# Performance work log

Hardware: AMD Instinct MI355X
Metric: run time of the kernel (lower is better)

## Reference

```python
import jax, jax.numpy as jnp
import numpy as np

B, S, H = 4, 1024, 2048
E = 16            # num_experts
K = 2             # num_experts_per_token
I = 1024          # per-expert intermediate_dim
N_SHARED = 2
I_SHARED = I * N_SHARED
RATIO = 0.1       # shared_expert_ratio
EPS = 1e-9


def _swiglu(x, wg, wu, wd):
    # SwiGLU, bias=False: down( silu(gate(x)) * up(x) )
    return (jax.nn.silu(x @ wg) * (x @ wu)) @ wd


def setup_inputs() -> dict:
    key = jax.random.key(0)
    ks = jax.random.split(key, 9)
    scale = 0.02
    x = jax.random.normal(ks[0], (B, S, H), dtype=jnp.float32)
    centroids = jax.random.normal(ks[1], (E, H), dtype=jnp.float32)  # nn.Parameter(randn)
    gate_bias = jnp.zeros((E,), dtype=jnp.float32)
    # shared expert SwiGLU weights (intermediate = I * n_shared_experts)
    wg_s = jax.random.normal(ks[2], (H, I_SHARED), dtype=jnp.float32) * scale
    wu_s = jax.random.normal(ks[3], (H, I_SHARED), dtype=jnp.float32) * scale
    wd_s = jax.random.normal(ks[4], (I_SHARED, H), dtype=jnp.float32) * scale
    # routed experts, stacked [E, ...]
    wg = jax.random.normal(ks[5], (E, H, I), dtype=jnp.float32) * scale
    wu = jax.random.normal(ks[6], (E, H, I), dtype=jnp.float32) * scale
    wd = jax.random.normal(ks[7], (E, I, H), dtype=jnp.float32) * scale
    return {"x": x, "centroids": centroids, "gate_bias": gate_bias,
            "wg_s": wg_s, "wu_s": wu_s, "wd_s": wd_s,
            "wg": wg, "wu": wu, "wd": wd}


def reference(x, centroids, gate_bias, wg_s, wu_s, wd_s, wg, wu, wd):
    # 1) shared expert on ALL tokens, scaled by ratio
    shared = _swiglu(x, wg_s, wu_s, wd_s) * RATIO          # [B,S,H]
    # 2) centroid affinity (DeepSeek-V3 sigmoid gating)
    affinity = jax.nn.sigmoid(jnp.einsum('bsh,eh->bse', x, centroids))  # [B,S,E]
    # 3) bias used ONLY for selection
    biased = affinity + gate_bias
    _, top_idx = jax.lax.top_k(biased, K)                  # [B,S,K]
    # 4) clean weights from unbiased affinity, normalized to sum 1
    top_aff = jnp.take_along_axis(affinity, top_idx, axis=-1)  # [B,S,K]
    weights = top_aff / (top_aff.sum(-1, keepdims=True) + EPS)
    # 5) combine-mask: per-token per-expert weight (0 if not selected)
    mask = (jax.nn.one_hot(top_idx, E, dtype=x.dtype) * weights[..., None]).sum(-2)  # [B,S,E]
    # 6) expert compute + weighted combine; loop over fixed small E avoids
    #    materializing a [B,S,E,H] tensor
    routed = jnp.zeros_like(x)
    for e in range(E):
        routed = routed + mask[..., e:e + 1] * _swiglu(x, wg[e], wu[e], wd[e])
    return shared + routed
```

## Files before the change

kernel.cpp:

```cpp
#include <hip/hip_runtime.h>
#include <hip/hip_bf16.h>

typedef unsigned short u16;
typedef unsigned int u32;
typedef unsigned long long u64;
typedef __attribute__((ext_vector_type(8))) short short8;
typedef __attribute__((ext_vector_type(4))) float f32x4;

#define TOKENS 4096
#define HDIM 2048
#define NEXP 16
#define IDIM 1024
#define ISH 2048
#define MAXTILES 80
#define NCHUNK 128

#define AS1(p) ((const __attribute__((address_space(1))) u32*)(p))
#define AS3(p) ((__attribute__((address_space(3))) u32*)(p))

__device__ __forceinline__ u16 f2b(float f) {
    u32 u = __float_as_uint(f);
    u32 r = u + 0x7fffu + ((u >> 16) & 1u);
    return (u16)(r >> 16);
}

__global__ __launch_bounds__(256) void convert_x_kernel(const float* __restrict__ x,
                                                        u16* __restrict__ xb) {
    size_t i = ((size_t)blockIdx.x * 256 + threadIdx.x) * 8;
    float4 a = *(const float4*)(x + i);
    float4 b = *(const float4*)(x + i + 4);
    u32 p0 = (u32)f2b(a.x) | ((u32)f2b(a.y) << 16);
    u32 p1 = (u32)f2b(a.z) | ((u32)f2b(a.w) << 16);
    u32 p2 = (u32)f2b(b.x) | ((u32)f2b(b.y) << 16);
    u32 p3 = (u32)f2b(b.z) | ((u32)f2b(b.w) << 16);
    uint4 o = make_uint4(p0, p1, p2, p3);
    *(uint4*)(xb + i) = o;
}

__global__ __launch_bounds__(256) void route_kernel(const float* __restrict__ x,
                                                    const float* __restrict__ cent,
                                                    const float* __restrict__ bias,
                                                    int* __restrict__ top_e,
                                                    float* __restrict__ top_w) {
    __shared__ alignas(16) float cs[8 * 2048];
    int lane = threadIdx.x & 63;
    int wv = threadIdx.x >> 6;
    int t = blockIdx.x * 4 + wv;
    const float4* xp4 = (const float4*)(x + (size_t)t * HDIM);
    float4 xr[8];
#pragma unroll
    for (int i = 0; i < 8; i++) xr[i] = xp4[lane + 64 * i];
    float aff[16];
#pragma unroll
    for (int ph = 0; ph < 2; ph++) {
        if (ph) __syncthreads();
        const float* sbase = cent + (size_t)(ph * 8 + wv * 2) * HDIM;
        float* dbase = cs + (size_t)wv * 2 * HDIM;
#pragma unroll
        for (int i = 0; i < 16; i++) {
            __builtin_amdgcn_global_load_lds(AS1(sbase + i * 256 + lane * 4),
                                             AS3(dbase + i * 256), 16, 0, 0);
        }
        __syncthreads();
#pragma unroll
        for (int e = 0; e < 8; e++) {
            const float4* cp = (const float4*)cs + (size_t)e * 512;
            float s = 0.f;
#pragma unroll
            for (int i = 0; i < 8; i++) {
                float4 cv = cp[lane + 64 * i];
                s += xr[i].x * cv.x;
                s += xr[i].y * cv.y;
                s += xr[i].z * cv.z;
                s += xr[i].w * cv.w;
            }
#pragma unroll
            for (int off = 32; off > 0; off >>= 1) s += __shfl_xor(s, off, 64);
            aff[ph * 8 + e] = 1.f / (1.f + expf(-s));
        }
    }
    float b0 = -1e30f, b1 = -1e30f, a0 = 0.f, a1 = 0.f;
    int e0 = -1, e1 = -1;
#pragma unroll
    for (int e = 0; e < 16; e++) {
        float v = aff[e] + bias[e];
        if (v > b0) {
            b1 = b0; e1 = e0; a1 = a0;
            b0 = v; e0 = e; a0 = aff[e];
        } else if (v > b1) {
            b1 = v; e1 = e; a1 = aff[e];
        }
    }
    float inv = 1.f / (a0 + a1 + 1e-9f);
    if (lane == 0) {
        top_e[2 * t] = e0; top_w[2 * t] = a0 * inv;
        top_e[2 * t + 1] = e1; top_w[2 * t + 1] = a1 * inv;
    }
}

__global__ __launch_bounds__(1024) void build_kernel(
    const int* __restrict__ top_e, const float* __restrict__ top_w,
    int* __restrict__ counts, int* __restrict__ offsets, int* __restrict__ ntiles,
    int* __restrict__ tile_e, int* __restrict__ tile_m,
    int* __restrict__ list_tok, float* __restrict__ list_w) {
    __shared__ int cnt[NCHUNK][16];
    __shared__ int offs_s[16];
    __shared__ int totals[16];
    int tid = threadIdx.x;
    int lane = tid & 63, wv = tid >> 6;
    for (int c = wv; c < NCHUNK; c += 16) {
        int v = top_e[c * 64 + lane];
#pragma unroll
        for (int e = 0; e < 16; e++) {
            u64 m = __ballot(v == e);
            if (lane == 0) cnt[c][e] = (int)__popcll(m);
        }
    }
    __syncthreads();
    if (tid < 16) {
        int s = 0;
        for (int c = 0; c < NCHUNK; c++) s += cnt[c][tid];
        totals[tid] = s;
        counts[tid] = s;
    }
    __syncthreads();
    if (tid == 0) {
        int r = 0, nt = 0;
        for (int e = 0; e < 16; e++) {
            offs_s[e] = r;
            offsets[e] = r;
            int ce = totals[e];
            int tcnt = (ce + 127) >> 7;
            for (int m = 0; m < tcnt; m++) {
                tile_e[nt] = e;
                tile_m[nt] = m;
                nt++;
            }
            r += ce;
        }
        *ntiles = nt;
    }
    __syncthreads();
    if (tid < 16) {
        int r = offs_s[tid];
        for (int c = 0; c < NCHUNK; c++) {
            int v = cnt[c][tid];
            cnt[c][tid] = r;
            r += v;
        }
    }
    __syncthreads();
    for (int c = wv; c < NCHUNK; c += 16) {
        int i = c * 64 + lane;
        int v = top_e[i];
        int rank = 0;
#pragma unroll
        for (int e = 0; e < 16; e++) {
            u64 m = __ballot(v == e);
            if (v == e) rank = (int)__popcll(m & ((1ull << lane) - 1ull));
        }
        int slot = cnt[c][v] + rank;
        list_tok[slot] = i >> 1;
        list_w[slot] = top_w[i];
    }
}

__global__ __launch_bounds__(256) void conv_w_kernel(const float* __restrict__ W,
                                                     u16* __restrict__ Wt, int K, int N) {
    int nt = blockIdx.x, kc = blockIdx.y;
    size_t mato = (size_t)blockIdx.z * K * N;
    const float* Wm = W + mato;
    u16* Wtm = Wt + mato;
    int ksB = K >> 5;
    __shared__ u16 Ls[64 * 40];
    int t = threadIdx.x;
    int kr = t >> 3, ng = t & 7;
    int nn = t >> 2, seg = t & 3;
    int g = seg ^ ((nn >> 2) & 3);
#pragma unroll
    for (int s = 0; s < 8; s++) {
        int kb = kc * 256 + s * 32;
        const float* src = Wm + (size_t)(kb + kr) * N + nt * 64 + ng * 8;
        float4 f0 = *(const float4*)src;
        float4 f1 = *(const float4*)(src + 4);
        __syncthreads();
        const float* p0 = (const float*)&f0;
        const float* p1 = (const float*)&f1;
#pragma unroll
        for (int l = 0; l < 4; l++) Ls[(8 * ng + l) * 40 + kr] = f2b(p0[l]);
#pragma unroll
        for (int l = 0; l < 4; l++) Ls[(8 * ng + 4 + l) * 40 + kr] = f2b(p1[l]);
        __syncthreads();
        const u16* lp = &Ls[nn * 40 + g * 8];
        u32 w0 = (u32)lp[0] | ((u32)lp[1] << 16);
        u32 w1 = (u32)lp[2] | ((u32)lp[3] << 16);
        u32 w2 = (u32)lp[4] | ((u32)lp[5] << 16);
        u32 w3 = (u32)lp[6] | ((u32)lp[7] << 16);
        uint4 o = make_uint4(w0, w1, w2, w3);
        *(uint4*)(Wtm + (size_t)(nt * ksB + (kb >> 5)) * 2048 + t * 8) = o;
    }
}

__global__ __launch_bounds__(256) void gemm_gateup(
    const u16* __restrict__ A, const u16* __restrict__ BgAll, const u16* __restrict__ BuAll,
    u16* __restrict__ hout, int Kd, int Nout, const int* __restrict__ counts,
    const int* __restrict__ offsets, const int* __restrict__ ntiles,
    const int* __restrict__ tile_e, const int* __restrict__ tile_m,
    const int* __restrict__ list_tok, int routed) {
    int cnt = TOKENS, base = 0, m0;
    const u16* Bg = BgAll;
    const u16* Bu = BuAll;
    if (routed) {
        int ti = blockIdx.x;
        if (ti >= *ntiles) return;
        int e = tile_e[ti];
        m0 = tile_m[ti] * 128;
        cnt = counts[e];
        base = offsets[e];
        size_t off = (size_t)e * Kd * Nout;
        Bg += off; Bu += off;
    } else {
        m0 = blockIdx.x * 128;
    }
    int nk = Kd >> 5;
    __shared__ alignas(16) u16 As[3][128 * 32];
    __shared__ alignas(16) u16 Bgs[3][64 * 32];
    __shared__ alignas(16) u16 Bus[3][64 * 32];
    int tid = threadIdx.x;
    int lane = tid & 63, wv = tid >> 6;
    int quad = lane >> 4, mr = lane & 15;
    int n0 = blockIdx.y * 64;
    int gk = (tid & 3) ^ ((tid >> 4) & 3);
    int mg0 = min(m0 + (tid >> 2), cnt - 1);
    int mg1 = min(m0 + 64 + (tid >> 2), cnt - 1);
    size_t sr0 = routed ? (size_t)list_tok[base + mg0] : (size_t)mg0;
    size_t sr1 = routed ? (size_t)list_tok[base + mg1] : (size_t)mg1;
    const u16* ap0 = A + sr0 * Kd + gk * 8;
    const u16* ap1 = A + sr1 * Kd + gk * 8;
    const u16* bgp = Bg + (size_t)blockIdx.y * nk * 2048 + tid * 8;
    const u16* bup = Bu + (size_t)blockIdx.y * nk * 2048 + tid * 8;
    int xq = quad ^ ((mr >> 2) & 3);
    f32x4 accg[2][4], accu[2][4];
#pragma unroll
    for (int i = 0; i < 2; i++)
#pragma unroll
        for (int j = 0; j < 4; j++) { accg[i][j] = (f32x4)0.f; accu[i][j] = (f32x4)0.f; }

#define STAGE_GU(b)                                                                     \
    do {                                                                                \
        __builtin_amdgcn_global_load_lds(AS1(ap0), AS3(&As[b][wv * 512]), 16, 0, 0);    \
        __builtin_amdgcn_global_load_lds(AS1(ap1), AS3(&As[b][2048 + wv * 512]), 16, 0, \
                                         0);                                            \
        __builtin_amdgcn_global_load_lds(AS1(bgp), AS3(&Bgs[b][wv * 512]), 16, 0, 0);   \
        __builtin_amdgcn_global_load_lds(AS1(bup), AS3(&Bus[b][wv * 512]), 16, 0, 0);   \
        ap0 += 32; ap1 += 32; bgp += 2048; bup += 2048;                                 \
    } while (0)

    STAGE_GU(0);
    STAGE_GU(1);
    asm volatile("s_waitcnt vmcnt(4)" ::: "memory");
    __builtin_amdgcn_s_barrier();

    int cur = 0;
    for (int ks = 0; ks < nk; ks++) {
        int nxt = cur + 2;
        if (nxt >= 3) nxt -= 3;
        if (ks + 2 < nk) STAGE_GU(nxt);
        const u16* Asc = As[cur];
        const u16* Bgc = Bgs[cur];
        const u16* Buc = Bus[cur];
        short8 a0 = *(const short8*)(Asc + ((32 * wv + mr) * 4 + xq) * 8);
        short8 a1 = *(const short8*)(Asc + ((32 * wv + 16 + mr) * 4 + xq) * 8);
#pragma unroll
        for (int j = 0; j < 4; j++) {
            short8 bg = *(const short8*)(Bgc + (64 * j + mr * 4 + xq) * 8);
            short8 bu = *(const short8*)(Buc + (64 * j + mr * 4 + xq) * 8);
            accg[0][j] = __builtin_amdgcn_mfma_f32_16x16x32_bf16(a0, bg, accg[0][j], 0, 0, 0);
            accg[1][j] = __builtin_amdgcn_mfma_f32_16x16x32_bf16(a1, bg, accg[1][j], 0, 0, 0);
            accu[0][j] = __builtin_amdgcn_mfma_f32_16x16x32_bf16(a0, bu, accu[0][j], 0, 0, 0);
            accu[1][j] = __builtin_amdgcn_mfma_f32_16x16x32_bf16(a1, bu, accu[1][j], 0, 0, 0);
        }
        if (ks + 2 < nk)
            asm volatile("s_waitcnt vmcnt(4)" ::: "memory");
        else
            asm volatile("s_waitcnt vmcnt(0)" ::: "memory");
        __builtin_amdgcn_s_barrier();
        cur = cur + 1 == 3 ? 0 : cur + 1;
    }
#undef STAGE_GU

#pragma unroll
    for (int i = 0; i < 2; i++)
#pragma unroll
        for (int j = 0; j < 4; j++)
#pragma unroll
            for (int r = 0; r < 4; r++) {
                int m = m0 + 32 * wv + 16 * i + quad * 4 + r;
                if (m < cnt) {
                    float gv = accg[i][j][r], uv = accu[i][j][r];
                    float h = gv / (1.f + expf(-gv)) * uv;
                    int n = n0 + 16 * j + mr;
                    hout[(size_t)(base + m) * Nout + n] = f2b(h);
                }
            }
}

__global__ __launch_bounds__(256) void gemm_down(
    const u16* __restrict__ A, const u16* __restrict__ BAll, float* __restrict__ out,
    int Kd, const int* __restrict__ counts, const int* __restrict__ offsets,
    const int* __restrict__ ntiles, const int* __restrict__ tile_e,
    const int* __restrict__ tile_m, const int* __restrict__ list_tok,
    const float* __restrict__ list_w, int routed) {
    int cnt = TOKENS, base = 0, m0;
    const u16* B = BAll;
    if (routed) {
        int ti = blockIdx.x;
        if (ti >= *ntiles) return;
        int e = tile_e[ti];
        m0 = tile_m[ti] * 128;
        cnt = counts[e];
        base = offsets[e];
        B += (size_t)e * Kd * HDIM;
    } else {
        m0 = blockIdx.x * 128;
    }
    int nk = Kd >> 5;
    __shared__ alignas(16) u16 As[3][128 * 32];
    __shared__ alignas(16) u16 Bs[3][64 * 32];
    int tid = threadIdx.x;
    int lane = tid & 63, wv = tid >> 6;
    int quad = lane >> 4, mr = lane & 15;
    int n0 = blockIdx.y * 64;
    int gk = (tid & 3) ^ ((tid >> 4) & 3);
    int mg0 = base + min(m0 + (tid >> 2), cnt - 1);
    int mg1 = base + min(m0 + 64 + (tid >> 2), cnt - 1);
    const u16* ap0 = A + (size_t)mg0 * Kd + gk * 8;
    const u16* ap1 = A + (size_t)mg1 * Kd + gk * 8;
    const u16* bp = B + (size_t)blockIdx.y * nk * 2048 + tid * 8;
    int xq = quad ^ ((mr >> 2) & 3);
    f32x4 acc[2][4];
#pragma unroll
    for (int i = 0; i < 2; i++)
#pragma unroll
        for (int j = 0; j < 4; j++) acc[i][j] = (f32x4)0.f;

#define STAGE_D(b)                                                                      \
    do {                                                                                \
        __builtin_amdgcn_global_load_lds(AS1(ap0), AS3(&As[b][wv * 512]), 16, 0, 0);    \
        __builtin_amdgcn_global_load_lds(AS1(ap1), AS3(&As[b][2048 + wv * 512]), 16, 0, \
                                         0);                                            \
        __builtin_amdgcn_global_load_lds(AS1(bp), AS3(&Bs[b][wv * 512]), 16, 0, 0);     \
        ap0 += 32; ap1 += 32; bp += 2048;                                               \
    } while (0)

    STAGE_D(0);
    STAGE_D(1);
    asm volatile("s_waitcnt vmcnt(3)" ::: "memory");
    __builtin_amdgcn_s_barrier();

    int cur = 0;
    for (int ks = 0; ks < nk; ks++) {
        int nxt = cur + 2;
        if (nxt >= 3) nxt -= 3;
        if (ks + 2 < nk) STAGE_D(nxt);
        const u16* Asc = As[cur];
        const u16* Bc = Bs[cur];
        short8 a0 = *(const short8*)(Asc + ((32 * wv + mr) * 4 + xq) * 8);
        short8 a1 = *(const short8*)(Asc + ((32 * wv + 16 + mr) * 4 + xq) * 8);
#pragma unroll
        for (int j = 0; j < 4; j++) {
            short8 b = *(const short8*)(Bc + (64 * j + mr * 4 + xq) * 8);
            acc[0][j] = __builtin_amdgcn_mfma_f32_16x16x32_bf16(a0, b, acc[0][j], 0, 0, 0);
            acc[1][j] = __builtin_amdgcn_mfma_f32_16x16x32_bf16(a1, b, acc[1][j], 0, 0, 0);
        }
        if (ks + 2 < nk)
            asm volatile("s_waitcnt vmcnt(3)" ::: "memory");
        else
            asm volatile("s_waitcnt vmcnt(0)" ::: "memory");
        __builtin_amdgcn_s_barrier();
        cur = cur + 1 == 3 ? 0 : cur + 1;
    }
#undef STAGE_D

#pragma unroll
    for (int i = 0; i < 2; i++)
#pragma unroll
        for (int j = 0; j < 4; j++)
#pragma unroll
            for (int r = 0; r < 4; r++) {
                int m = m0 + 32 * wv + 16 * i + quad * 4 + r;
                if (m >= cnt) continue;
                int n = n0 + 16 * j + mr;
                float v = acc[i][j][r];
                if (routed) {
                    int tok = list_tok[base + m];
                    atomicAdd(out + (size_t)tok * HDIM + n, list_w[base + m] * v);
                } else {
                    out[(size_t)m * HDIM + n] = 0.1f * v;
                }
            }
}

extern "C" void kernel_launch(void* const* d_in, const int* in_sizes, int n_in,
                              void* d_out, int out_size, void* d_ws, size_t ws_size,
                              hipStream_t stream) {
    const float* x = (const float*)d_in[0];
    const float* cent = (const float*)d_in[1];
    const float* bias = (const float*)d_in[2];
    const float* wgs = (const float*)d_in[3];
    const float* wus = (const float*)d_in[4];
    const float* wds = (const float*)d_in[5];
    const float* wg = (const float*)d_in[6];
    const float* wu = (const float*)d_in[7];
    const float* wd = (const float*)d_in[8];
    float* out = (float*)d_out;
    char* ws = (char*)d_ws;

    size_t off_wtgs = 0;
    size_t off_wtus = off_wtgs + (size_t)HDIM * ISH * 2;
    size_t off_wtds = off_wtus + (size_t)HDIM * ISH * 2;
    size_t off_wtg = off_wtds + (size_t)ISH * HDIM * 2;
    size_t off_wtu = off_wtg + (size_t)NEXP * HDIM * IDIM * 2;
    size_t off_wtd = off_wtu + (size_t)NEXP * HDIM * IDIM * 2;
    size_t off_xbf = off_wtd + (size_t)NEXP * IDIM * HDIM * 2;
    size_t off_hsh = off_xbf + (size_t)TOKENS * HDIM * 2;
    size_t off_hrt = off_hsh + (size_t)TOKENS * ISH * 2;
    size_t off_meta = off_hrt + (size_t)2 * TOKENS * IDIM * 2;
    size_t need = off_meta + (1 << 20);
    if (ws_size < need) return;

    u16* Wt_gs = (u16*)(ws + off_wtgs);
    u16* Wt_us = (u16*)(ws + off_wtus);
    u16* Wt_ds = (u16*)(ws + off_wtds);
    u16* Wt_g = (u16*)(ws + off_wtg);
    u16* Wt_u = (u16*)(ws + off_wtu);
    u16* Wt_d = (u16*)(ws + off_wtd);
    u16* x_bf = (u16*)(ws + off_xbf);
    u16* h_sh = (u16*)(ws + off_hsh);
    u16* h_rt = (u16*)(ws + off_hrt);
    int* counts = (int*)(ws + off_meta);
    int* offsets = counts + 16;
    int* ntiles = offsets + 16;
    int* tile_e = ntiles + 16;
    int* tile_m = tile_e + MAXTILES;
    int* top_e = tile_m + MAXTILES;
    int* top_s = top_e + 2 * TOKENS;
    float* top_w = (float*)(top_s + 2 * TOKENS);
    int* list_tok = (int*)(top_w + 2 * TOKENS);
    float* list_w = (float*)(list_tok + 2 * TOKENS);

    convert_x_kernel<<<TOKENS * HDIM / (256 * 8), 256, 0, stream>>>(x, x_bf);
    route_kernel<<<TOKENS / 4, 256, 0, stream>>>(x, cent, bias, top_e, top_w);
    build_kernel<<<1, 1024, 0, stream>>>(top_e, top_w, counts, offsets, ntiles, tile_e,
                                         tile_m, list_tok, list_w);

    conv_w_kernel<<<dim3(ISH / 64, HDIM / 256, 1), 256, 0, stream>>>(wgs, Wt_gs, HDIM, ISH);
    conv_w_kernel<<<dim3(ISH / 64, HDIM / 256, 1), 256, 0, stream>>>(wus, Wt_us, HDIM, ISH);
    conv_w_kernel<<<dim3(HDIM / 64, ISH / 256, 1), 256, 0, stream>>>(wds, Wt_ds, ISH, HDIM);
    conv_w_kernel<<<dim3(IDIM / 64, HDIM / 256, NEXP), 256, 0, stream>>>(wg, Wt_g, HDIM, IDIM);
    conv_w_kernel<<<dim3(IDIM / 64, HDIM / 256, NEXP), 256, 0, stream>>>(wu, Wt_u, HDIM, IDIM);
    conv_w_kernel<<<dim3(HDIM / 64, IDIM / 256, NEXP), 256, 0, stream>>>(wd, Wt_d, IDIM, HDIM);

    gemm_gateup<<<dim3(TOKENS / 128, ISH / 64, 1), 256, 0, stream>>>(
        x_bf, Wt_gs, Wt_us, h_sh, HDIM, ISH, nullptr, nullptr, nullptr, nullptr, nullptr,
        nullptr, 0);
    gemm_down<<<dim3(TOKENS / 128, HDIM / 64, 1), 256, 0, stream>>>(
        h_sh, Wt_ds, out, ISH, nullptr, nullptr, nullptr, nullptr, nullptr, nullptr, nullptr, 0);
    gemm_gateup<<<dim3(MAXTILES, IDIM / 64, 1), 256, 0, stream>>>(
        x_bf, Wt_g, Wt_u, h_rt, HDIM, IDIM, counts, offsets, ntiles, tile_e, tile_m,
        list_tok, 1);
    gemm_down<<<dim3(MAXTILES, HDIM / 64, 1), 256, 0, stream>>>(
        h_rt, Wt_d, out, IDIM, counts, offsets, ntiles, tile_e, tile_m, list_tok, list_w, 1);
}
```

Before: 1.005 ms.

## Use 256-row GEMM tiles and replace routed atomic scatter with a combine kernel

Doubles the M tile of the gate/up and down GEMMs from 128 to 256 rows, giving each wave 4x4 MFMA accumulators, and cuts MAXTILES to 48 to match. The LDS pipeline drops from triple buffering with explicit vmcnt waits to double buffering with __syncthreads. The routed down GEMM now writes unweighted per-slot rows into a scratch buffer instead of doing float atomicAdd into the output. A new combine kernel then applies the two routing weights per token using a tok2slot map built during routing. The aim is more B-operand reuse per tile and no atomic contention, at the cost of higher register pressure, a shallower load pipeline, and an extra pass over a 64 MB scratch buffer.

```diff
diff --git a/kernel.cpp b/kernel.cpp
--- a/kernel.cpp
+++ b/kernel.cpp
@@ -12,7 +12,7 @@
 #define NEXP 16
 #define IDIM 1024
 #define ISH 2048
-#define MAXTILES 80
+#define MAXTILES 48
 #define NCHUNK 128
 
 #define AS1(p) ((const __attribute__((address_space(1))) u32*)(p))
@@ -102,7 +102,8 @@
     const int* __restrict__ top_e, const float* __restrict__ top_w,
     int* __restrict__ counts, int* __restrict__ offsets, int* __restrict__ ntiles,
     int* __restrict__ tile_e, int* __restrict__ tile_m,
-    int* __restrict__ list_tok, float* __restrict__ list_w) {
+    int* __restrict__ list_tok, float* __restrict__ list_w,
+    int* __restrict__ tok2slot) {
     __shared__ int cnt[NCHUNK][16];
     __shared__ int offs_s[16];
     __shared__ int totals[16];
@@ -130,7 +131,7 @@
             offs_s[e] = r;
             offsets[e] = r;
             int ce = totals[e];
-            int tcnt = (ce + 127) >> 7;
+            int tcnt = (ce + 255) >> 8;
             for (int m = 0; m < tcnt; m++) {
                 tile_e[nt] = e;
                 tile_m[nt] = m;
@@ -162,6 +163,7 @@
         int slot = cnt[c][v] + rank;
         list_tok[slot] = i >> 1;
         list_w[slot] = top_w[i];
+        tok2slot[i] = slot;
     }
 }
 
@@ -214,88 +216,101 @@
         int ti = blockIdx.x;
         if (ti >= *ntiles) return;
         int e = tile_e[ti];
-        m0 = tile_m[ti] * 128;
+        m0 = tile_m[ti] * 256;
         cnt = counts[e];
         base = offsets[e];
         size_t off = (size_t)e * Kd * Nout;
         Bg += off; Bu += off;
     } else {
-        m0 = blockIdx.x * 128;
+        m0 = blockIdx.x * 256;
     }
     int nk = Kd >> 5;
-    __shared__ alignas(16) u16 As[3][128 * 32];
-    __shared__ alignas(16) u16 Bgs[3][64 * 32];
-    __shared__ alignas(16) u16 Bus[3][64 * 32];
+    __shared__ alignas(16) u16 As[2][256 * 32];
+    __shared__ alignas(16) u16 Bgs[2][64 * 32];
+    __shared__ alignas(16) u16 Bus[2][64 * 32];
     int tid = threadIdx.x;
     int lane = tid & 63, wv = tid >> 6;
     int quad = lane >> 4, mr = lane & 15;
     int n0 = blockIdx.y * 64;
     int gk = (tid & 3) ^ ((tid >> 4) & 3);
-    int mg0 = min(m0 + (tid >> 2), cnt - 1);
-    int mg1 = min(m0 + 64 + (tid >> 2), cnt - 1);
-    size_t sr0 = routed ? (size_t)list_tok[base + mg0] : (size_t)mg0;
-    size_t sr1 = routed ? (size_t)list_tok[base + mg1] : (size_t)mg1;
-    const u16* ap0 = A + sr0 * Kd + gk * 8;
-    const u16* ap1 = A + sr1 * Kd + gk * 8;
+    const u16* ap0;
+    const u16* ap1;
+    const u16* ap2;
+    const u16* ap3;
+    {
+        int mg0 = min(m0 + 0 * 64 + (tid >> 2), cnt - 1);
+        int mg1 = min(m0 + 1 * 64 + (tid >> 2), cnt - 1);
+        int mg2 = min(m0 + 2 * 64 + (tid >> 2), cnt - 1);
+        int mg3 = min(m0 + 3 * 64 + (tid >> 2), cnt - 1);
+        size_t s0 = routed ? (size_t)list_tok[base + mg0] : (size_t)mg0;
+        size_t s1 = routed ? (size_t)list_tok[base + mg1] : (size_t)mg1;
+        size_t s2 = routed ? (size_t)list_tok[base + mg2] : (size_t)mg2;
+        size_t s3 = routed ? (size_t)list_tok[base + mg3] : (size_t)mg3;
+        ap0 = A + s0 * Kd + gk * 8;
+        ap1 = A + s1 * Kd + gk * 8;
+        ap2 = A + s2 * Kd + gk * 8;
+        ap3 = A + s3 * Kd + gk * 8;
+    }
     const u16* bgp = Bg + (size_t)blockIdx.y * nk * 2048 + tid * 8;
     const u16* bup = Bu + (size_t)blockIdx.y * nk * 2048 + tid * 8;
     int xq = quad ^ ((mr >> 2) & 3);
-    f32x4 accg[2][4], accu[2][4];
-#pragma unroll
-    for (int i = 0; i < 2; i++)
+    f32x4 accg[4][4], accu[4][4];
+#pragma unroll
+    for (int i = 0; i < 4; i++)
 #pragma unroll
         for (int j = 0; j < 4; j++) { accg[i][j] = (f32x4)0.f; accu[i][j] = (f32x4)0.f; }
 
-#define STAGE_GU(b)                                                                     \
-    do {                                                                                \
-        __builtin_amdgcn_global_load_lds(AS1(ap0), AS3(&As[b][wv * 512]), 16, 0, 0);    \
-        __builtin_amdgcn_global_load_lds(AS1(ap1), AS3(&As[b][2048 + wv * 512]), 16, 0, \
-                                         0);                                            \
-        __builtin_amdgcn_global_load_lds(AS1(bgp), AS3(&Bgs[b][wv * 512]), 16, 0, 0);   \
-        __builtin_amdgcn_global_load_lds(AS1(bup), AS3(&Bus[b][wv * 512]), 16, 0, 0);   \
-        ap0 += 32; ap1 += 32; bgp += 2048; bup += 2048;                                 \
+#define STAGE_GU(b)                                                                       \
+    do {                                                                                  \
+        __builtin_amdgcn_global_load_lds(AS1(ap0), AS3(&As[b][0 + wv * 512]), 16, 0, 0);  \
+        __builtin_amdgcn_global_load_lds(AS1(ap1), AS3(&As[b][2048 + wv * 512]), 16, 0,   \
+                                         0);                                              \
+        __builtin_amdgcn_global_load_lds(AS1(ap2), AS3(&As[b][4096 + wv * 512]), 16, 0,   \
+                                         0);                                              \
+        __builtin_amdgcn_global_load_lds(AS1(ap3), AS3(&As[b][6144 + wv * 512]), 16, 0,   \
+                                         0);                                              \
+        __builtin_amdgcn_global_load_lds(AS1(bgp), AS3(&Bgs[b][wv * 512]), 16, 0, 0);     \
+        __builtin_amdgcn_global_load_lds(AS1(bup), AS3(&Bus[b][wv * 512]), 16, 0, 0);     \
+        ap0 += 32; ap1 += 32; ap2 += 32; ap3 += 32; bgp += 2048; bup += 2048;             \
     } while (0)
 
     STAGE_GU(0);
-    STAGE_GU(1);
-    asm volatile("s_waitcnt vmcnt(4)" ::: "memory");
-    __builtin_amdgcn_s_barrier();
-
+    __syncthreads();
     int cur = 0;
     for (int ks = 0; ks < nk; ks++) {
-        int nxt = cur + 2;
-        if (nxt >= 3) nxt -= 3;
-        if (ks + 2 < nk) STAGE_GU(nxt);
+        if (ks + 1 < nk) STAGE_GU(cur ^ 1);
         const u16* Asc = As[cur];
         const u16* Bgc = Bgs[cur];
         const u16* Buc = Bus[cur];
-        short8 a0 = *(const short8*)(Asc + ((32 * wv + mr) * 4 + xq) * 8);
-        short8 a1 = *(const short8*)(Asc + ((32 * wv + 16 + mr) * 4 + xq) * 8);
+        short8 a0 = *(const short8*)(Asc + ((64 * wv + 0 + mr) * 4 + xq) * 8);
+        short8 a1 = *(const short8*)(Asc + ((64 * wv + 16 + mr) * 4 + xq) * 8);
+        short8 a2 = *(const short8*)(Asc + ((64 * wv + 32 + mr) * 4 + xq) * 8);
+        short8 a3 = *(const short8*)(Asc + ((64 * wv + 48 + mr) * 4 + xq) * 8);
 #pragma unroll
         for (int j = 0; j < 4; j++) {
-            short8 bg = *(const short8*)(Bgc + (64 * j + mr * 4 + xq) * 8);
-            short8 bu = *(const short8*)(Buc + (64 * j + mr * 4 + xq) * 8);
+            short8 bg = *(const short8*)(Bgc + ((16 * j + mr) * 4 + xq) * 8);
+            short8 bu = *(const short8*)(Buc + ((16 * j + mr) * 4 + xq) * 8);
             accg[0][j] = __builtin_amdgcn_mfma_f32_16x16x32_bf16(a0, bg, accg[0][j], 0, 0, 0);
             accg[1][j] = __builtin_amdgcn_mfma_f32_16x16x32_bf16(a1, bg, accg[1][j], 0, 0, 0);
+            accg[2][j] = __builtin_amdgcn_mfma_f32_16x16x32_bf16(a2, bg, accg[2][j], 0, 0, 0);
+            accg[3][j] = __builtin_amdgcn_mfma_f32_16x16x32_bf16(a3, bg, accg[3][j], 0, 0, 0);
             accu[0][j] = __builtin_amdgcn_mfma_f32_16x16x32_bf16(a0, bu, accu[0][j], 0, 0, 0);
             accu[1][j] = __builtin_amdgcn_mfma_f32_16x16x32_bf16(a1, bu, accu[1][j], 0, 0, 0);
-        }
-        if (ks + 2 < nk)
-            asm volatile("s_waitcnt vmcnt(4)" ::: "memory");
-        else
-            asm volatile("s_waitcnt vmcnt(0)" ::: "memory");
-        __builtin_amdgcn_s_barrier();
-        cur = cur + 1 == 3 ? 0 : cur + 1;
+            accu[2][j] = __builtin_amdgcn_mfma_f32_16x16x32_bf16(a2, bu, accu[2][j], 0, 0, 0);
+            accu[3][j] = __builtin_amdgcn_mfma_f32_16x16x32_bf16(a3, bu, accu[3][j], 0, 0, 0);
+        }
+        __syncthreads();
+        cur ^= 1;
     }
 #undef STAGE_GU
 
 #pragma unroll
-    for (int i = 0; i < 2; i++)
+    for (int i = 0; i < 4; i++)
 #pragma unroll
         for (int j = 0; j < 4; j++)
 #pragma unroll
             for (int r = 0; r < 4; r++) {
-                int m = m0 + 32 * wv + 16 * i + quad * 4 + r;
+                int m = m0 + 64 * wv + 16 * i + quad * 4 + r;
                 if (m < cnt) {
                     float gv = accg[i][j][r], uv = accu[i][j][r];
                     float h = gv / (1.f + expf(-gv)) * uv;
@@ -306,99 +321,130 @@
 }
 
 __global__ __launch_bounds__(256) void gemm_down(
-    const u16* __restrict__ A, const u16* __restrict__ BAll, float* __restrict__ out,
+    const u16* __restrict__ A, const u16* __restrict__ BAll, float* __restrict__ outp,
     int Kd, const int* __restrict__ counts, const int* __restrict__ offsets,
     const int* __restrict__ ntiles, const int* __restrict__ tile_e,
-    const int* __restrict__ tile_m, const int* __restrict__ list_tok,
-    const float* __restrict__ list_w, int routed) {
+    const int* __restrict__ tile_m, const int* __restrict__ list_tok, int routed) {
     int cnt = TOKENS, base = 0, m0;
     const u16* B = BAll;
     if (routed) {
         int ti = blockIdx.x;
         if (ti >= *ntiles) return;
         int e = tile_e[ti];
-        m0 = tile_m[ti] * 128;
+        m0 = tile_m[ti] * 256;
         cnt = counts[e];
         base = offsets[e];
         B += (size_t)e * Kd * HDIM;
     } else {
-        m0 = blockIdx.x * 128;
+        m0 = blockIdx.x * 256;
     }
     int nk = Kd >> 5;
-    __shared__ alignas(16) u16 As[3][128 * 32];
-    __shared__ alignas(16) u16 Bs[3][64 * 32];
+    __shared__ alignas(16) u16 As[2][256 * 32];
+    __shared__ alignas(16) u16 Bs[2][64 * 32];
     int tid = threadIdx.x;
     int lane = tid & 63, wv = tid >> 6;
     int quad = lane >> 4, mr = lane & 15;
     int n0 = blockIdx.y * 64;
     int gk = (tid & 3) ^ ((tid >> 4) & 3);
-    int mg0 = base + min(m0 + (tid >> 2), cnt - 1);
-    int mg1 = base + min(m0 + 64 + (tid >> 2), cnt - 1);
-    const u16* ap0 = A + (size_t)mg0 * Kd + gk * 8;
-    const u16* ap1 = A + (size_t)mg1 * Kd + gk * 8;
+    const u16* ap0;
+    const u16* ap1;
+    const u16* ap2;
+    const u16* ap3;
+    {
+        int mg0 = base + min(m0 + 0 * 64 + (tid >> 2), cnt - 1);
+        int mg1 = base + min(m0 + 1 * 64 + (tid >> 2), cnt - 1);
+        int mg2 = base + min(m0 + 2 * 64 + (tid >> 2), cnt - 1);
+        int mg3 = base + min(m0 + 3 * 64 + (tid >> 2), cnt - 1);
+        ap0 = A + (size_t)mg0 * Kd + gk * 8;
+        ap1 = A + (size_t)mg1 * Kd + gk * 8;
+        ap2 = A + (size_t)mg2 * Kd + gk * 8;
+        ap3 = A + (size_t)mg3 * Kd + gk * 8;
+    }
     const u16* bp = B + (size_t)blockIdx.y * nk * 2048 + tid * 8;
     int xq = quad ^ ((mr >> 2) & 3);
-    f32x4 acc[2][4];
-#pragma unroll
-    for (int i = 0; i < 2; i++)
+    f32x4 acc[4][4];
+#pragma unroll
+    for (int i = 0; i < 4; i++)
 #pragma unroll
         for (int j = 0; j < 4; j++) acc[i][j] = (f32x4)0.f;
 
-#define STAGE_D(b)                                                                      \
-    do {                                                                                \
-        __builtin_amdgcn_global_load_lds(AS1(ap0), AS3(&As[b][wv * 512]), 16, 0, 0);    \
-        __builtin_amdgcn_global_load_lds(AS1(ap1), AS3(&As[b][2048 + wv * 512]), 16, 0, \
-                                         0);                                            \
-        __builtin_amdgcn_global_load_lds(AS1(bp), AS3(&Bs[b][wv * 512]), 16, 0, 0);     \
-        ap0 += 32; ap1 += 32; bp += 2048;                                               \
+#define STAGE_D(b)                                                                        \
+    do {                                                                                  \
+        __builtin_amdgcn_global_load_lds(AS1(ap0), AS3(&As[b][0 + wv * 512]), 16, 0, 0);  \
+        __builtin_amdgcn_global_load_lds(AS1(ap1), AS3(&As[b][2048 + wv * 512]), 16, 0,   \
+                                         0);                                              \
+        __builtin_amdgcn_global_load_lds(AS1(ap2), AS3(&As[b][4096 + wv * 512]), 16, 0,   \
+                                         0);                                              \
+        __builtin_amdgcn_global_load_lds(AS1(ap3), AS3(&As[b][6144 + wv * 512]), 16, 0,   \
+                                         0);                                              \
+        __builtin_amdgcn_global_load_lds(AS1(bp), AS3(&Bs[b][wv * 512]), 16, 0, 0);       \
+        ap0 += 32; ap1 += 32; ap2 += 32; ap3 += 32; bp += 2048;                           \
     } while (0)
 
     STAGE_D(0);
-    STAGE_D(1);
-    asm volatile("s_waitcnt vmcnt(3)" ::: "memory");
-    __builtin_amdgcn_s_barrier();
-
+    __syncthreads();
     int cur = 0;
     for (int ks = 0; ks < nk; ks++) {
-        int nxt = cur + 2;
-        if (nxt >= 3) nxt -= 3;
-        if (ks + 2 < nk) STAGE_D(nxt);
+        if (ks + 1 < nk) STAGE_D(cur ^ 1);
         const u16* Asc = As[cur];
         const u16* Bc = Bs[cur];
-        short8 a0 = *(const short8*)(Asc + ((32 * wv + mr) * 4 + xq) * 8);
-        short8 a1 = *(const short8*)(Asc + ((32 * wv + 16 + mr) * 4 + xq) * 8);
+        short8 a0 = *(const short8*)(Asc + ((64 * wv + 0 + mr) * 4 + xq) * 8);
+        short8 a1 = *(const short8*)(Asc + ((64 * wv + 16 + mr) * 4 + xq) * 8);
+        short8 a2 = *(const short8*)(Asc + ((64 * wv + 32 + mr) * 4 + xq) * 8);
+        short8 a3 = *(const short8*)(Asc + ((64 * wv + 48 + mr) * 4 + xq) * 8);
 #pragma unroll
         for (int j = 0; j < 4; j++) {
-            short8 b = *(const short8*)(Bc + (64 * j + mr * 4 + xq) * 8);
+            short8 b = *(const short8*)(Bc + ((16 * j + mr) * 4 + xq) * 8);
             acc[0][j] = __builtin_amdgcn_mfma_f32_16x16x32_bf16(a0, b, acc[0][j], 0, 0, 0);
             acc[1][j] = __builtin_amdgcn_mfma_f32_16x16x32_bf16(a1, b, acc[1][j], 0, 0, 0);
-        }
-        if (ks + 2 < nk)
-            asm volatile("s_waitcnt vmcnt(3)" ::: "memory");
-        else
-            asm volatile("s_waitcnt vmcnt(0)" ::: "memory");
-        __builtin_amdgcn_s_barrier();
-        cur = cur + 1 == 3 ? 0 : cur + 1;
+            acc[2][j] = __builtin_amdgcn_mfma_f32_16x16x32_bf16(a2, b, acc[2][j], 0, 0, 0);
+            acc[3][j] = __builtin_amdgcn_mfma_f32_16x16x32_bf16(a3, b, acc[3][j], 0, 0, 0);
+        }
+        __syncthreads();
+        cur ^= 1;
     }
 #undef STAGE_D
 
 #pragma unroll
-    for (int i = 0; i < 2; i++)
+    for (int i = 0; i < 4; i++)
 #pragma unroll
         for (int j = 0; j < 4; j++)
 #pragma unroll
             for (int r = 0; r < 4; r++) {
-                int m = m0 + 32 * wv + 16 * i + quad * 4 + r;
+                int m = m0 + 64 * wv + 16 * i + quad * 4 + r;
                 if (m >= cnt) continue;
                 int n = n0 + 16 * j + mr;
                 float v = acc[i][j][r];
                 if (routed) {
-                    int tok = list_tok[base + m];
-                    atomicAdd(out + (size_t)tok * HDIM + n, list_w[base + m] * v);
+                    outp[(size_t)(base + m) * HDIM + n] = v;
                 } else {
-                    out[(size_t)m * HDIM + n] = 0.1f * v;
+                    outp[(size_t)m * HDIM + n] = 0.1f * v;
                 }
             }
+}
+
+__global__ __launch_bounds__(256) void combine_kernel(float* __restrict__ out,
+                                                      const float* __restrict__ rd,
+                                                      const int* __restrict__ tok2slot,
+                                                      const float* __restrict__ top_w) {
+    int t = blockIdx.x;
+    int s0 = tok2slot[2 * t], s1 = tok2slot[2 * t + 1];
+    float w0 = top_w[2 * t], w1 = top_w[2 * t + 1];
+    const float4* r0 = (const float4*)(rd + (size_t)s0 * HDIM);
+    const float4* r1 = (const float4*)(rd + (size_t)s1 * HDIM);
+    float4* op = (float4*)(out + (size_t)t * HDIM);
+#pragma unroll
+    for (int k = 0; k < 2; k++) {
+        int c = threadIdx.x + k * 256;
+        float4 o = op[c];
+        float4 a = r0[c];
+        float4 b = r1[c];
+        o.x += w0 * a.x + w1 * b.x;
+        o.y += w0 * a.y + w1 * b.y;
+        o.z += w0 * a.z + w1 * b.z;
+        o.w += w0 * a.w + w1 * b.w;
+        op[c] = o;
+    }
 }
 
 extern "C" void kernel_launch(void* const* d_in, const int* in_sizes, int n_in,
@@ -438,21 +484,22 @@
     u16* x_bf = (u16*)(ws + off_xbf);
     u16* h_sh = (u16*)(ws + off_hsh);
     u16* h_rt = (u16*)(ws + off_hrt);
+    float* rd = (float*)ws;
     int* counts = (int*)(ws + off_meta);
     int* offsets = counts + 16;
     int* ntiles = offsets + 16;
     int* tile_e = ntiles + 16;
     int* tile_m = tile_e + MAXTILES;
-    int* top_e = tile_m + MAXTILES;
-    int* top_s = top_e + 2 * TOKENS;
-    float* top_w = (float*)(top_s + 2 * TOKENS);
+    int* tok2slot = tile_m + MAXTILES;
+    int* top_e = tok2slot + 2 * TOKENS;
+    float* top_w = (float*)(top_e + 2 * TOKENS);
     int* list_tok = (int*)(top_w + 2 * TOKENS);
     float* list_w = (float*)(list_tok + 2 * TOKENS);
 
     convert_x_kernel<<<TOKENS * HDIM / (256 * 8), 256, 0, stream>>>(x, x_bf);
     route_kernel<<<TOKENS / 4, 256, 0, stream>>>(x, cent, bias, top_e, top_w);
     build_kernel<<<1, 1024, 0, stream>>>(top_e, top_w, counts, offsets, ntiles, tile_e,
-                                         tile_m, list_tok, list_w);
+                                         tile_m, list_tok, list_w, tok2slot);
 
     conv_w_kernel<<<dim3(ISH / 64, HDIM / 256, 1), 256, 0, stream>>>(wgs, Wt_gs, HDIM, ISH);
     conv_w_kernel<<<dim3(ISH / 64, HDIM / 256, 1), 256, 0, stream>>>(wus, Wt_us, HDIM, ISH);
@@ -461,14 +508,15 @@
     conv_w_kernel<<<dim3(IDIM / 64, HDIM / 256, NEXP), 256, 0, stream>>>(wu, Wt_u, HDIM, IDIM);
     conv_w_kernel<<<dim3(HDIM / 64, IDIM / 256, NEXP), 256, 0, stream>>>(wd, Wt_d, IDIM, HDIM);
 
-    gemm_gateup<<<dim3(TOKENS / 128, ISH / 64, 1), 256, 0, stream>>>(
+    gemm_gateup<<<dim3(TOKENS / 256, ISH / 64, 1), 256, 0, stream>>>(
         x_bf, Wt_gs, Wt_us, h_sh, HDIM, ISH, nullptr, nullptr, nullptr, nullptr, nullptr,
         nullptr, 0);
-    gemm_down<<<dim3(TOKENS / 128, HDIM / 64, 1), 256, 0, stream>>>(
-        h_sh, Wt_ds, out, ISH, nullptr, nullptr, nullptr, nullptr, nullptr, nullptr, nullptr, 0);
+    gemm_down<<<dim3(TOKENS / 256, HDIM / 64, 1), 256, 0, stream>>>(
+        h_sh, Wt_ds, out, ISH, nullptr, nullptr, nullptr, nullptr, nullptr, nullptr, 0);
     gemm_gateup<<<dim3(MAXTILES, IDIM / 64, 1), 256, 0, stream>>>(
         x_bf, Wt_g, Wt_u, h_rt, HDIM, IDIM, counts, offsets, ntiles, tile_e, tile_m,
         list_tok, 1);
     gemm_down<<<dim3(MAXTILES, HDIM / 64, 1), 256, 0, stream>>>(
-        h_rt, Wt_d, out, IDIM, counts, offsets, ntiles, tile_e, tile_m, list_tok, list_w, 1);
-}
+        h_rt, Wt_d, rd, IDIM, counts, offsets, ntiles, tile_e, tile_m, list_tok, 1);
+    combine_kernel<<<TOKENS, 256, 0, stream>>>(out, rd, tok2slot, top_w);
+}
```

Measured after the change: 1.084 ms. +7.9%, slower.
